# Kernel optimization log

Hardware: AMD Instinct MI355X
Metric: run time of the kernel (lower is better)

Reference implementation:

```python
import jax, jax.numpy as jnp
import numpy as np

# --- model constants (match init_kwargs / Mamba2 defaults) ---
NUM_BLOCKS = 2
D_MODEL = 768
EXPAND = 2
D_INNER = EXPAND * D_MODEL          # 1536
D_STATE = 128
D_CONV = 4
HEADDIM = 64
NHEADS = D_INNER // HEADDIM         # 24
CONV_DIM = D_INNER + 2 * D_STATE    # 1792 (x, B, C go through the depthwise conv)
D_IN_PROJ = 2 * D_INNER + 2 * D_STATE + NHEADS  # 3352
VOCAB = 32000
LABEL_DIM = 1000
EPS = 1e-5


def _layernorm(x, w, b):
    mu = jnp.mean(x, axis=-1, keepdims=True)
    var = jnp.mean(jnp.square(x - mu), axis=-1, keepdims=True)
    return (x - mu) * jax.lax.rsqrt(var + EPS) * w + b


def _dwconv_causal(x, w, b):
    # x: [B, L, C], w: [C, K] depthwise kernel, b: [C]
    C, K = w.shape
    xt = jnp.transpose(x, (0, 2, 1))  # [B, C, L]
    out = jax.lax.conv_general_dilated(
        xt, w[:, None, :], window_strides=(1,), padding=[(K - 1, 0)],
        feature_group_count=C, dimension_numbers=("NCH", "OIH", "NCH"))
    return jnp.transpose(out, (0, 2, 1)) + b


def _ssd_scan(xh, Bm, Cm, dt, A):
    # xh: [B,L,H,P], Bm/Cm: [B,L,N], dt: [B,L,H], A: [H]
    Bsz, L, H, P = xh.shape
    N = Bm.shape[-1]
    dA = jnp.exp(dt * A)  # [B,L,H], in (0,1)

    def step(h, inp):
        xt, bt, ct, dat, dtt = inp  # [B,H,P],[B,N],[B,N],[B,H],[B,H]
        h = h * dat[:, :, None, None] + (dtt[:, :, None, None] * xt[..., None]) * bt[:, None, None, :]
        y = jnp.einsum('bhpn,bn->bhp', h, ct)
        return h, y

    h0 = jnp.zeros((Bsz, H, P, N), dtype=xh.dtype)
    xs = (jnp.transpose(xh, (1, 0, 2, 3)),
          jnp.transpose(Bm, (1, 0, 2)),
          jnp.transpose(Cm, (1, 0, 2)),
          jnp.transpose(dA, (1, 0, 2)),
          jnp.transpose(dt, (1, 0, 2)))
    _, ys = jax.lax.scan(step, h0, xs)  # ys: [L,B,H,P]
    return jnp.transpose(ys, (1, 0, 2, 3))


def _mamba2(x, Win, conv_w, conv_b, dt_bias, A_log, Dp, rms_w, Wout):
    Bsz, L, _ = x.shape
    zxbcdt = x @ Win  # [B,L,D_IN_PROJ]
    z = zxbcdt[..., :D_INNER]
    xBC = zxbcdt[..., D_INNER:D_INNER + CONV_DIM]
    dt = zxbcdt[..., D_INNER + CONV_DIM:]  # [B,L,H]
    dt = jax.nn.softplus(dt + dt_bias)

    xBC = jax.nn.silu(_dwconv_causal(xBC, conv_w, conv_b))
    xs = xBC[..., :D_INNER]
    Bm = xBC[..., D_INNER:D_INNER + D_STATE]
    Cm = xBC[..., D_INNER + D_STATE:]

    xh = xs.reshape(Bsz, L, NHEADS, HEADDIM)
    A = -jnp.exp(A_log)  # [H]
    y = _ssd_scan(xh, Bm, Cm, dt, A) + Dp[None, None, :, None] * xh  # [B,L,H,P]
    y = y.reshape(Bsz, L, D_INNER)

    # gated RMSNorm: norm(y * silu(z)) * weight
    y = y * jax.nn.silu(z)
    y = y * jax.lax.rsqrt(jnp.mean(jnp.square(y), axis=-1, keepdims=True) + EPS) * rms_w
    return y @ Wout


def _forward(tokens, emb, ln_w, ln_b, Win, conv_w, conv_b, dt_bias, A_log, Dp, rms_w, Wout, Wcls, bcls):
    x = emb[tokens]  # [B,L,D_MODEL]
    for i in range(NUM_BLOCKS):
        nx = _layernorm(x, ln_w[i], ln_b[i])
        x = x + _mamba2(nx, Win[i], conv_w[i], conv_b[i], dt_bias[i],
                        A_log[i], Dp[i], rms_w[i], Wout[i])
        # dropout_rate=0 (eval) -> identity; use_glu=False -> no post stage
    return x @ Wcls + bcls


def setup_inputs() -> dict:
    key = jax.random.key(0)
    ks = jax.random.split(key, 12)
    B, L = 2, 512
    tokens = jax.random.randint(ks[0], (B, L), 0, VOCAB)
    emb = jax.random.normal(ks[1], (VOCAB, D_MODEL), jnp.float32) * 0.02
    ln_w = jnp.ones((NUM_BLOCKS, D_MODEL), jnp.float32)
    ln_b = jnp.zeros((NUM_BLOCKS, D_MODEL), jnp.float32)
    Win = jax.random.normal(ks[2], (NUM_BLOCKS, D_MODEL, D_IN_PROJ), jnp.float32) / np.sqrt(D_MODEL)
    conv_w = jax.random.normal(ks[3], (NUM_BLOCKS, CONV_DIM, D_CONV), jnp.float32) / np.sqrt(D_CONV)
    conv_b = jnp.zeros((NUM_BLOCKS, CONV_DIM), jnp.float32)
    dt0 = jax.random.uniform(ks[4], (NUM_BLOCKS, NHEADS), jnp.float32, 1e-3, 0.1)
    dt_bias = dt0 + jnp.log(-jnp.expm1(-dt0))  # inverse softplus
    A_log = jnp.log(jax.random.uniform(ks[5], (NUM_BLOCKS, NHEADS), jnp.float32, 1.0, 16.0))
    Dp = jnp.ones((NUM_BLOCKS, NHEADS), jnp.float32)
    rms_w = jnp.ones((NUM_BLOCKS, D_INNER), jnp.float32)
    Wout = jax.random.normal(ks[6], (NUM_BLOCKS, D_INNER, D_MODEL), jnp.float32) / np.sqrt(D_INNER)
    Wcls = jax.random.normal(ks[7], (D_MODEL, LABEL_DIM), jnp.float32) / np.sqrt(D_MODEL)
    bcls = jnp.zeros((LABEL_DIM,), jnp.float32)
    return {"tokens": tokens, "emb": emb, "ln_w": ln_w, "ln_b": ln_b, "Win": Win,
            "conv_w": conv_w, "conv_b": conv_b, "dt_bias": dt_bias, "A_log": A_log,
            "Dp": Dp, "rms_w": rms_w, "Wout": Wout, "Wcls": Wcls, "bcls": bcls}


def reference(tokens, emb, ln_w, ln_b, Win, conv_w, conv_b, dt_bias, A_log, Dp, rms_w, Wout, Wcls, bcls):
    return _forward(tokens, emb, ln_w, ln_b, Win, conv_w, conv_b, dt_bias, A_log, Dp, rms_w, Wout, Wcls, bcls)
```

## Files before the change

kernel.cpp:

```cpp
#include <hip/hip_runtime.h>
#include <hip/hip_bf16.h>
#include <math.h>

#define B_SZ 2
#define L_SEQ 512
#define DMODEL 768
#define DINNER 1536
#define DSTATE 128
#define HEADDIM 64
#define NHEADS 24
#define CONVDIM 1792
#define DINPROJ 3352
#define ROWS (B_SZ * L_SEQ)

#define CHUNK 32
#define NCHUNK (L_SEQ / CHUNK)
#define BCDIM (2 * DSTATE)

#define NPAD_IN 3456
#define NPAD_CLS 1024

typedef __attribute__((ext_vector_type(8))) __bf16 bf16x8;
typedef __attribute__((ext_vector_type(4))) __bf16 bf16x4;
typedef __attribute__((ext_vector_type(4))) float f32x4;

typedef __attribute__((address_space(1))) const unsigned int as1_u32;
typedef __attribute__((address_space(3))) unsigned int as3_u32;

__device__ __forceinline__ void gload16(const void* g, void* s) {
  __builtin_amdgcn_global_load_lds((as1_u32*)(unsigned long)g, (as3_u32*)(unsigned long)s, 16, 0,
                                   0);
}

__device__ __forceinline__ float siluf(float x) { return x / (1.f + expf(-x)); }
__device__ __forceinline__ float softplusf(float x) {
  return x > 0.f ? x + log1pf(expf(-x)) : log1pf(expf(x));
}

__device__ __forceinline__ float block_reduce_sum(float v, float* sred) {
  int tid = threadIdx.x;
  for (int off = 32; off; off >>= 1) v += __shfl_down(v, off, 64);
  int wid = tid >> 6, lane = tid & 63;
  if (lane == 0) sred[wid] = v;
  __syncthreads();
  float total;
  if (tid == 0) {
    total = 0.f;
    int nw = blockDim.x >> 6;
    for (int i = 0; i < nw; ++i) total += sred[i];
    sred[0] = total;
  }
  __syncthreads();
  total = sred[0];
  __syncthreads();
  return total;
}

__global__ __launch_bounds__(256) void decomp_all_kernel(
    const float* __restrict__ Win, const float* __restrict__ Wout,
    const float* __restrict__ Wcls, const int* __restrict__ tok, const float* __restrict__ emb,
    const float* __restrict__ lnw0, const float* __restrict__ lnb0, float* __restrict__ x,
    __bf16* __restrict__ nxh, __bf16* __restrict__ nxl, __bf16* __restrict__ wih0,
    __bf16* __restrict__ wil0, __bf16* __restrict__ wih1, __bf16* __restrict__ wil1,
    __bf16* __restrict__ woh0, __bf16* __restrict__ wol0, __bf16* __restrict__ woh1,
    __bf16* __restrict__ wol1, __bf16* __restrict__ wch, __bf16* __restrict__ wcl) {
  constexpr int TIN = (NPAD_IN / 32) * (DMODEL / 32);
  constexpr int TOUT = (DMODEL / 32) * (DINNER / 32);
  constexpr int TCLS = (NPAD_CLS / 32) * (DMODEL / 32);
  __shared__ float tile[32][33];
  int bid = blockIdx.x;
  int tid = threadIdx.x;

  if (bid >= 2 * TIN + 2 * TOUT + TCLS) {
    int row = bid - (2 * TIN + 2 * TOUT + TCLS);
    int t = tok[row];
    float v[3];
    float s = 0.f;
#pragma unroll
    for (int j = 0; j < 3; ++j) {
      v[j] = emb[(size_t)t * DMODEL + tid + j * 256];
      s += v[j];
      x[(size_t)row * DMODEL + tid + j * 256] = v[j];
    }
    float* sred = (float*)tile;
    float mean = block_reduce_sum(s, sred) * (1.f / DMODEL);
    float s2 = 0.f;
#pragma unroll
    for (int j = 0; j < 3; ++j) {
      float d = v[j] - mean;
      s2 += d * d;
    }
    float var = block_reduce_sum(s2, sred) * (1.f / DMODEL);
    float r = 1.f / sqrtf(var + 1e-5f);
#pragma unroll
    for (int j = 0; j < 3; ++j) {
      int d = tid + j * 256;
      float val = (v[j] - mean) * r * lnw0[d] + lnb0[d];
      __bf16 h = (__bf16)val;
      nxh[(size_t)row * DMODEL + d] = h;
      nxl[(size_t)row * DMODEL + d] = (__bf16)(val - (float)h);
    }
    return;
  }

  const float* W;
  __bf16 *Th, *Tl;
  int K, N, ntx, r;
  if (bid < TIN) {
    W = Win; Th = wih0; Tl = wil0; K = DMODEL; N = DINPROJ; ntx = NPAD_IN / 32; r = bid;
  } else if (bid < 2 * TIN) {
    W = Win + (size_t)DMODEL * DINPROJ; Th = wih1; Tl = wil1; K = DMODEL; N = DINPROJ;
    ntx = NPAD_IN / 32; r = bid - TIN;
  } else if (bid < 2 * TIN + TOUT) {
    W = Wout; Th = woh0; Tl = wol0; K = DINNER; N = DMODEL; ntx = DMODEL / 32; r = bid - 2 * TIN;
  } else if (bid < 2 * TIN + 2 * TOUT) {
    W = Wout + (size_t)DINNER * DMODEL; Th = woh1; Tl = wol1; K = DINNER; N = DMODEL;
    ntx = DMODEL / 32; r = bid - 2 * TIN - TOUT;
  } else {
    W = Wcls; Th = wch; Tl = wcl; K = DMODEL; N = 1000; ntx = NPAD_CLS / 32;
    r = bid - 2 * TIN - 2 * TOUT;
  }
  int bn = (r % ntx) * 32, bk = (r / ntx) * 32;

  int i = tid >> 3, j4 = (tid & 7) * 4;
  int kk = bk + i;
  int nn = bn + j4;
  float4 v;
  if (nn + 3 < N) {
    v = *(const float4*)(W + (size_t)kk * N + nn);
  } else {
    v.x = (nn + 0 < N) ? W[(size_t)kk * N + nn + 0] : 0.f;
    v.y = (nn + 1 < N) ? W[(size_t)kk * N + nn + 1] : 0.f;
    v.z = (nn + 2 < N) ? W[(size_t)kk * N + nn + 2] : 0.f;
    v.w = (nn + 3 < N) ? W[(size_t)kk * N + nn + 3] : 0.f;
  }
  tile[i][j4 + 0] = v.x;
  tile[i][j4 + 1] = v.y;
  tile[i][j4 + 2] = v.z;
  tile[i][j4 + 3] = v.w;
  __syncthreads();
  int n = bn + i;
  bf16x4 hv, lv;
#pragma unroll
  for (int q = 0; q < 4; ++q) {
    float f = tile[j4 + q][i];
    __bf16 h = (__bf16)f;
    hv[q] = h;
    lv[q] = (__bf16)(f - (float)h);
  }
  *(bf16x4*)(Th + (size_t)n * K + bk + j4) = hv;
  *(bf16x4*)(Tl + (size_t)n * K + bk + j4) = lv;
}

__global__ __launch_bounds__(256) void ln_kernel(const float* __restrict__ x,
                                                 const float* __restrict__ w,
                                                 const float* __restrict__ b,
                                                 __bf16* __restrict__ oh,
                                                 __bf16* __restrict__ ol) {
  __shared__ float sred[8];
  int row = blockIdx.x, tid = threadIdx.x;
  const float* xr = x + (size_t)row * DMODEL;
  float v[3];
  float s = 0.f;
#pragma unroll
  for (int j = 0; j < 3; ++j) {
    v[j] = xr[tid + j * 256];
    s += v[j];
  }
  float mean = block_reduce_sum(s, sred) * (1.f / DMODEL);
  float s2 = 0.f;
#pragma unroll
  for (int j = 0; j < 3; ++j) {
    float d = v[j] - mean;
    s2 += d * d;
  }
  float var = block_reduce_sum(s2, sred) * (1.f / DMODEL);
  float r = 1.f / sqrtf(var + 1e-5f);
#pragma unroll
  for (int j = 0; j < 3; ++j) {
    int d = tid + j * 256;
    float val = (v[j] - mean) * r * w[d] + b[d];
    __bf16 h = (__bf16)val;
    oh[(size_t)row * DMODEL + d] = h;
    ol[(size_t)row * DMODEL + d] = (__bf16)(val - (float)h);
  }
}

__global__ __launch_bounds__(256) void act_decomp_kernel(const float* __restrict__ x,
                                                         __bf16* __restrict__ oh,
                                                         __bf16* __restrict__ ol) {
  int row = blockIdx.x, tid = threadIdx.x;
#pragma unroll
  for (int j = 0; j < 3; ++j) {
    int d = tid + j * 256;
    float v = x[(size_t)row * DMODEL + d];
    __bf16 h = (__bf16)v;
    oh[(size_t)row * DMODEL + d] = h;
    ol[(size_t)row * DMODEL + d] = (__bf16)(v - (float)h);
  }
}

template <int FM, int FN, bool ATOMIC>
__global__ __launch_bounds__(256) void mfma_gemm_kernel(
    const __bf16* __restrict__ Ahi, const __bf16* __restrict__ Alo,
    const __bf16* __restrict__ Bhi, const __bf16* __restrict__ Blo,
    const float* __restrict__ addsrc, const float* __restrict__ bias, float* __restrict__ C,
    int N, int K, int kslice, int nbx, int nwg) {
  constexpr int BM = FM * 32;
  constexpr int BN = FN * 32;
  constexpr int RGA = BM / 16;
  constexpr int RGB = BN / 16;
  constexpr int NITER = (2 * (RGA + RGB)) / 4;
  constexpr int ABYTES = BM * 64;
  constexpr int BBYTES = BN * 64;
  constexpr int BUFBYTES = 2 * ABYTES + 2 * BBYTES;
  __shared__ char lds[2 * BUFBYTES];

  int tid = threadIdx.x;
  int wave = tid >> 6, lane = tid & 63;
  int wm = wave >> 1, wn = wave & 1;
  int bx, by;
  if (nbx > 0) {
    int orig = (blockIdx.x % 8) * (nwg / 8) + blockIdx.x / 8;
    bx = orig % nbx;
    by = orig / nbx;
  } else {
    bx = blockIdx.x;
    by = blockIdx.y;
  }
  int bm = by * BM;
  int bn = bx * BN;
  int kbeg = ATOMIC ? blockIdx.z * kslice : 0;
  int kend = ATOMIC ? (kbeg + kslice) : K;
  int l2 = lane >> 2;
  int gch = (lane & 3) ^ ((lane >> 3) & 3);
  int lr = lane & 15, lg = lane >> 4;

  f32x4 acc[FM][FN] = {};

  auto stage = [&](char* buf, int k0) {
#pragma unroll
    for (int it = 0; it < NITER; ++it) {
      int rg = wave + it * 4;
      const __bf16* src;
      int row0, boff;
      if (rg < RGA) {
        src = Ahi;
        row0 = bm + rg * 16;
        boff = rg * 1024;
      } else if (rg < 2 * RGA) {
        src = Alo;
        row0 = bm + (rg - RGA) * 16;
        boff = ABYTES + (rg - RGA) * 1024;
      } else if (rg < 2 * RGA + RGB) {
        src = Bhi;
        row0 = bn + (rg - 2 * RGA) * 16;
        boff = 2 * ABYTES + (rg - 2 * RGA) * 1024;
      } else {
        src = Blo;
        row0 = bn + (rg - 2 * RGA - RGB) * 16;
        boff = 2 * ABYTES + BBYTES + (rg - 2 * RGA - RGB) * 1024;
      }
      gload16(src + (size_t)(row0 + l2) * K + k0 + gch * 8, buf + boff);
    }
  };

  stage(lds, kbeg);
  __syncthreads();

  char* curb = lds;
  char* nxtb = lds + BUFBYTES;
  for (int k0 = kbeg; k0 < kend; k0 += 32) {
    if (k0 + 32 < kend) stage(nxtb, k0 + 32);

    bf16x8 ahi[FM], alo[FM], bhi[FN], blo[FN];
#pragma unroll
    for (int m = 0; m < FM; ++m) {
      int r = wm * FM * 16 + m * 16 + lr;
      int off = r * 64 + ((lg ^ ((r >> 1) & 3)) * 16);
      ahi[m] = *(const bf16x8*)(curb + off);
      alo[m] = *(const bf16x8*)(curb + ABYTES + off);
    }
#pragma unroll
    for (int n = 0; n < FN; ++n) {
      int r = wn * FN * 16 + n * 16 + lr;
      int off = r * 64 + ((lg ^ ((r >> 1) & 3)) * 16);
      bhi[n] = *(const bf16x8*)(curb + 2 * ABYTES + off);
      blo[n] = *(const bf16x8*)(curb + 2 * ABYTES + BBYTES + off);
    }
#pragma unroll
    for (int m = 0; m < FM; ++m)
#pragma unroll
      for (int n = 0; n < FN; ++n) {
        acc[m][n] = __builtin_amdgcn_mfma_f32_16x16x32_bf16(ahi[m], bhi[n], acc[m][n], 0, 0, 0);
        acc[m][n] = __builtin_amdgcn_mfma_f32_16x16x32_bf16(ahi[m], blo[n], acc[m][n], 0, 0, 0);
        acc[m][n] = __builtin_amdgcn_mfma_f32_16x16x32_bf16(alo[m], bhi[n], acc[m][n], 0, 0, 0);
      }
    __syncthreads();
    char* t = curb;
    curb = nxtb;
    nxtb = t;
  }

#pragma unroll
  for (int m = 0; m < FM; ++m) {
#pragma unroll
    for (int n = 0; n < FN; ++n) {
      int gcol = bn + wn * FN * 16 + n * 16 + lr;
      if (gcol < N) {
#pragma unroll
        for (int r = 0; r < 4; ++r) {
          int grow = bm + wm * FM * 16 + m * 16 + lg * 4 + r;
          if (ATOMIC) {
            unsafeAtomicAdd(&C[(size_t)grow * N + gcol], acc[m][n][r]);
          } else {
            float v = acc[m][n][r];
            if (addsrc) v += addsrc[(size_t)grow * N + gcol];
            if (bias) v += bias[gcol];
            C[(size_t)grow * N + gcol] = v;
          }
        }
      }
    }
  }
}

__global__ __launch_bounds__(256) void convBC_kernel(const float* __restrict__ zx,
                                                     const float* __restrict__ cw,
                                                     const float* __restrict__ cb,
                                                     const float* __restrict__ dtb,
                                                     float* __restrict__ xBC,
                                                     float* __restrict__ dts) {
  int row = blockIdx.x;
  int c = threadIdx.x;
  int ch = DINNER + c;
  int l = row & (L_SEQ - 1);
  float acc = cb[ch];
#pragma unroll
  for (int k = 0; k < 4; ++k) {
    int ls = l - 3 + k;
    if (ls >= 0)
      acc = fmaf(cw[ch * 4 + k], zx[(size_t)(row - 3 + k) * DINPROJ + DINNER + ch], acc);
  }
  xBC[(size_t)row * BCDIM + c] = siluf(acc);
  if (c < NHEADS) {
    float raw = zx[(size_t)row * DINPROJ + DINNER + CONVDIM + c] + dtb[c];
    dts[(size_t)row * NHEADS + c] = softplusf(raw);
  }
}

__global__ __launch_bounds__(256) void sraw_kernel(const float* __restrict__ xBC,
                                                   float* __restrict__ Sraw) {
  __shared__ float Bs[CHUNK][132];
  __shared__ float Cs[CHUNK][132];
  int ci = blockIdx.x, b = blockIdx.y;
  int tid = threadIdx.x;
  int row0 = b * L_SEQ + ci * CHUNK;
#pragma unroll
  for (int i = 0; i < 4; ++i) {
    int vi = tid + i * 256;
    int t = vi >> 5;
    int n4 = (vi & 31) * 4;
    const float* r = xBC + (size_t)(row0 + t) * BCDIM;
    *(float4*)&Bs[t][n4] = *(const float4*)(r + n4);
    *(float4*)&Cs[t][n4] = *(const float4*)(r + DSTATE + n4);
  }
  __syncthreads();
  int t0 = (tid >> 4) * 2;
  int s0 = (tid & 15) * 2;
  float sacc[2][2] = {};
#pragma unroll
  for (int n = 0; n < DSTATE; n += 4) {
    float cr[2][4], br[2][4];
#pragma unroll
    for (int i = 0; i < 2; ++i) *(float4*)&cr[i][0] = *(const float4*)&Cs[t0 + i][n];
#pragma unroll
    for (int j = 0; j < 2; ++j) *(float4*)&br[j][0] = *(const float4*)&Bs[s0 + j][n];
#pragma unroll
    for (int i = 0; i < 2; ++i)
#pragma unroll
      for (int j = 0; j < 2; ++j)
#pragma unroll
        for (int k = 0; k < 4; ++k) sacc[i][j] = fmaf(cr[i][k], br[j][k], sacc[i][j]);
  }
  float* Sp = Sraw + ((size_t)(b * NCHUNK + ci) * CHUNK) * CHUNK;
#pragma unroll
  for (int i = 0; i < 2; ++i)
#pragma unroll
    for (int j = 0; j < 2; ++j) Sp[(t0 + i) * CHUNK + s0 + j] = sacc[i][j];
}

__global__ __launch_bounds__(256) void chunk_local_kernel(
    const float* __restrict__ zx, const float* __restrict__ xBC, const float* __restrict__ Sraw,
    const float* __restrict__ dts, const float* __restrict__ cw, const float* __restrict__ cb,
    const float* __restrict__ Alog, const float* __restrict__ Dp, float* __restrict__ y,
    __bf16* __restrict__ G, float* __restrict__ et, float* __restrict__ elast) {
  __shared__ float Bs[CHUNK][132];
  __shared__ float Xs[CHUNK][68];
  __shared__ float Ss[CHUNK][36];
  __shared__ float sP[CHUNK], sW[CHUNK], sDt[CHUNK];

  int ci = blockIdx.x, h = blockIdx.y, b = blockIdx.z;
  int bh = b * NHEADS + h;
  int tid = threadIdx.x;
  int row0 = b * L_SEQ + ci * CHUNK;

#pragma unroll
  for (int i = 0; i < 2; ++i) {
    int vi = tid + i * 256;
    int t = vi >> 4;
    int n8 = (vi & 15) * 8;
    const float* r = xBC + (size_t)(row0 + t) * BCDIM;
    *(float4*)&Bs[t][n8] = *(const float4*)(r + n8);
    *(float4*)&Bs[t][n8 + 4] = *(const float4*)(r + n8 + 4);
  }
#pragma unroll
  for (int i = 0; i < 2; ++i) {
    int vi = tid + i * 256;
    int t = vi >> 4;
    int p4 = (vi & 15) * 4;
    int cX = h * HEADDIM + p4;
    float oX[4];
#pragma unroll
    for (int q = 0; q < 4; ++q) oX[q] = cb[cX + q];
#pragma unroll
    for (int k = 0; k < 4; ++k) {
      if (ci > 0 || t + k >= 3) {
        float4 v = *(const float4*)(zx + (size_t)(row0 + t - 3 + k) * DINPROJ + DINNER + cX);
#pragma unroll
        for (int q = 0; q < 4; ++q) oX[q] = fmaf(cw[(cX + q) * 4 + k], ((const float*)&v)[q], oX[q]);
      }
    }
#pragma unroll
    for (int q = 0; q < 4; ++q) Xs[t][p4 + q] = siluf(oX[q]);
  }
  if (tid < 32) {
    int t = tid;
    float Ah = -expf(Alog[h]);
    float dtv = dts[(size_t)(row0 + t) * NHEADS + h];
    float P = dtv * Ah;
#pragma unroll
    for (int off = 1; off < 32; off <<= 1) {
      float u = __shfl_up(P, off, 32);
      if (t >= off) P += u;
    }
    float Plast = __shfl(P, 31, 32);
    float e = expf(P);
    sP[t] = P;
    sDt[t] = dtv;
    sW[t] = expf(Plast - P) * dtv;
    et[(size_t)(bh * NCHUNK + ci) * CHUNK + t] = e;
    if (t == 31) elast[bh * NCHUNK + ci] = e;
  }
  __syncthreads();

  int t0 = (tid >> 4) * 2;
  int s0 = (tid & 15) * 2;
  {
    const float* Sp = Sraw + ((size_t)(b * NCHUNK + ci) * CHUNK) * CHUNK;
#pragma unroll
    for (int i = 0; i < 2; ++i)
#pragma unroll
      for (int j = 0; j < 2; ++j) {
        int t = t0 + i, s = s0 + j;
        float sr = Sp[t * CHUNK + s];
        Ss[t][s] = (t >= s) ? sr * expf(sP[t] - sP[s]) * sDt[s] : 0.f;
      }
  }
  __syncthreads();

  {
    int p0 = (tid & 15) * 4;
    float acc[2][4] = {};
#pragma unroll
    for (int s = 0; s < CHUNK; s += 4) {
      float sr[2][4], xr[4][4];
#pragma unroll
      for (int i = 0; i < 2; ++i) *(float4*)&sr[i][0] = *(const float4*)&Ss[t0 + i][s];
#pragma unroll
      for (int u = 0; u < 4; ++u) *(float4*)&xr[u][0] = *(const float4*)&Xs[s + u][p0];
#pragma unroll
      for (int i = 0; i < 2; ++i)
#pragma unroll
        for (int j = 0; j < 4; ++j)
#pragma unroll
          for (int u = 0; u < 4; ++u) acc[i][j] = fmaf(sr[i][u], xr[u][j], acc[i][j]);
    }
    float Dh = Dp[h];
#pragma unroll
    for (int i = 0; i < 2; ++i) {
      int row = row0 + t0 + i;
      float4 o;
      o.x = acc[i][0] + Dh * Xs[t0 + i][p0 + 0];
      o.y = acc[i][1] + Dh * Xs[t0 + i][p0 + 1];
      o.z = acc[i][2] + Dh * Xs[t0 + i][p0 + 2];
      o.w = acc[i][3] + Dh * Xs[t0 + i][p0 + 3];
      *(float4*)(y + (size_t)row * DINNER + h * HEADDIM + p0) = o;
    }
  }

  {
    int n0 = (tid >> 4) * 8;
    int p0 = (tid & 15) * 4;
    float g[8][4] = {};
#pragma unroll 4
    for (int s = 0; s < CHUNK; ++s) {
      float w = sW[s];
      float bv[8], xv[4];
      *(float4*)&bv[0] = *(const float4*)&Bs[s][n0];
      *(float4*)&bv[4] = *(const float4*)&Bs[s][n0 + 4];
      *(float4*)&xv[0] = *(const float4*)&Xs[s][p0];
#pragma unroll
      for (int k = 0; k < 8; ++k) {
        float wb = w * bv[k];
#pragma unroll
        for (int j = 0; j < 4; ++j) g[k][j] = fmaf(wb, xv[j], g[k][j]);
      }
    }
    __bf16* Gp = G + ((size_t)bh * NCHUNK + ci) * (DSTATE * HEADDIM);
#pragma unroll
    for (int k = 0; k < 8; ++k) {
      bf16x4 o;
#pragma unroll
      for (int q = 0; q < 4; ++q) o[q] = (__bf16)g[k][q];
      *(bf16x4*)(Gp + (size_t)(n0 + k) * HEADDIM + p0) = o;
    }
  }
}

__global__ __launch_bounds__(256) void combine_kernel(__bf16* __restrict__ G,
                                                      const float* __restrict__ elast) {
  int part = blockIdx.x;
  int bh = blockIdx.y;
  int gi = part * 256 + threadIdx.x;
  __bf16* base = G + (size_t)bh * NCHUNK * (DSTATE * HEADDIM);
  const float* el = elast + bh * NCHUNK;
  float h0 = 0.f, h1 = 0.f, h2 = 0.f, h3 = 0.f;
#pragma unroll
  for (int c = 0; c < NCHUNK - 1; ++c) {
    bf16x4 g = *(bf16x4*)(base + (size_t)c * (DSTATE * HEADDIM) + gi * 4);
    float e = el[c];
    h0 = fmaf(e, h0, (float)g[0]);
    h1 = fmaf(e, h1, (float)g[1]);
    h2 = fmaf(e, h2, (float)g[2]);
    h3 = fmaf(e, h3, (float)g[3]);
    bf16x4 o;
    o[0] = (__bf16)h0;
    o[1] = (__bf16)h1;
    o[2] = (__bf16)h2;
    o[3] = (__bf16)h3;
    *(bf16x4*)(base + (size_t)c * (DSTATE * HEADDIM) + gi * 4) = o;
  }
}

__global__ __launch_bounds__(256) void apply_inter_kernel(const float* __restrict__ xBC,
                                                          const __bf16* __restrict__ G,
                                                          const float* __restrict__ et,
                                                          float* __restrict__ y) {
  __shared__ float Cs[CHUNK][132];
  __shared__ float Hs[DSTATE][68];
  __shared__ float sE[CHUNK];
  int ci = blockIdx.x + 1;
  int h = blockIdx.y, b = blockIdx.z;
  int bh = b * NHEADS + h;
  int tid = threadIdx.x;
  int row0 = b * L_SEQ + ci * CHUNK;

#pragma unroll
  for (int i = 0; i < 4; ++i) {
    int vi = tid + i * 256;
    int t = vi >> 5;
    int n4 = (vi & 31) * 4;
    *(float4*)&Cs[t][n4] = *(const float4*)(xBC + (size_t)(row0 + t) * BCDIM + DSTATE + n4);
  }
  const __bf16* Hsrc = G + ((size_t)bh * NCHUNK + (ci - 1)) * (DSTATE * HEADDIM);
#pragma unroll
  for (int i = 0; i < 8; ++i) {
    int vi = tid + i * 256;
    int n = vi >> 4;
    int p4 = (vi & 15) * 4;
    bf16x4 g = *(const bf16x4*)(Hsrc + (size_t)n * HEADDIM + p4);
#pragma unroll
    for (int q = 0; q < 4; ++q) Hs[n][p4 + q] = (float)g[q];
  }
  if (tid < CHUNK) sE[tid] = et[(size_t)(bh * NCHUNK + ci) * CHUNK + tid];
  __syncthreads();

  int t0 = (tid >> 4) * 2;
  int p0 = (tid & 15) * 4;
  float acc[2][4] = {};
#pragma unroll
  for (int n = 0; n < DSTATE; n += 4) {
    float cr[2][4], hr[4][4];
#pragma unroll
    for (int i = 0; i < 2; ++i) *(float4*)&cr[i][0] = *(const float4*)&Cs[t0 + i][n];
#pragma unroll
    for (int u = 0; u < 4; ++u) *(float4*)&hr[u][0] = *(const float4*)&Hs[n + u][p0];
#pragma unroll
    for (int i = 0; i < 2; ++i)
#pragma unroll
      for (int j = 0; j < 4; ++j)
#pragma unroll
        for (int u = 0; u < 4; ++u) acc[i][j] = fmaf(cr[i][u], hr[u][j], acc[i][j]);
  }
#pragma unroll
  for (int i = 0; i < 2; ++i) {
    int row = row0 + t0 + i;
    float e = sE[t0 + i];
    float* yp = y + (size_t)row * DINNER + h * HEADDIM + p0;
    float4 cur = *(float4*)yp;
    cur.x = fmaf(e, acc[i][0], cur.x);
    cur.y = fmaf(e, acc[i][1], cur.y);
    cur.z = fmaf(e, acc[i][2], cur.z);
    cur.w = fmaf(e, acc[i][3], cur.w);
    *(float4*)yp = cur;
  }
}

__global__ __launch_bounds__(256) void gate_rms_kernel(const float* __restrict__ y,
                                                       const float* __restrict__ zx,
                                                       const float* __restrict__ rmsw,
                                                       __bf16* __restrict__ oh,
                                                       __bf16* __restrict__ ol) {
  __shared__ float sred[8];
  int row = blockIdx.x, tid = threadIdx.x;
  const float* z = zx + (size_t)row * DINPROJ;
  const float* yr = y + (size_t)row * DINNER;
  float v[6];
  float ss = 0.f;
#pragma unroll
  for (int j = 0; j < 6; ++j) {
    int d = tid + j * 256;
    float val = yr[d] * siluf(z[d]);
    v[j] = val;
    ss += val * val;
  }
  float total = block_reduce_sum(ss, sred);
  float r = 1.f / sqrtf(total * (1.f / DINNER) + 1e-5f);
#pragma unroll
  for (int j = 0; j < 6; ++j) {
    int d = tid + j * 256;
    float val = v[j] * r * rmsw[d];
    __bf16 h = (__bf16)val;
    oh[(size_t)row * DINNER + d] = h;
    ol[(size_t)row * DINNER + d] = (__bf16)(val - (float)h);
  }
}

extern "C" void kernel_launch(void* const* d_in, const int* in_sizes, int n_in,
                              void* d_out, int out_size, void* d_ws, size_t ws_size,
                              hipStream_t stream) {
  const int* tokens = (const int*)d_in[0];
  const float* emb = (const float*)d_in[1];
  const float* ln_w = (const float*)d_in[2];
  const float* ln_b = (const float*)d_in[3];
  const float* Win = (const float*)d_in[4];
  const float* conv_w = (const float*)d_in[5];
  const float* conv_b = (const float*)d_in[6];
  const float* dt_bias = (const float*)d_in[7];
  const float* A_log = (const float*)d_in[8];
  const float* Dp = (const float*)d_in[9];
  const float* rms_w = (const float*)d_in[10];
  const float* Wout = (const float*)d_in[11];
  const float* Wcls = (const float*)d_in[12];
  const float* bcls = (const float*)d_in[13];
  float* out = (float*)d_out;

  float* ws = (float*)d_ws;
  float* x = ws;
  float* zx = x + (size_t)ROWS * DMODEL;
  float* y = zx + (size_t)ROWS * DINPROJ;
  __bf16* G = (__bf16*)(y + (size_t)ROWS * DINNER);
  float* et = (float*)(G + (size_t)B_SZ * NHEADS * NCHUNK * DSTATE * HEADDIM);
  float* elast = et + (size_t)B_SZ * NHEADS * NCHUNK * CHUNK;
  float* xBC = elast + B_SZ * NHEADS * NCHUNK;
  float* Sraw = xBC + (size_t)ROWS * BCDIM;
  float* dts = Sraw + (size_t)B_SZ * NCHUNK * CHUNK * CHUNK;
  __bf16* bp = (__bf16*)(dts + (size_t)ROWS * NHEADS);
  __bf16* nxh = bp;  bp += (size_t)ROWS * DMODEL;
  __bf16* nxl = bp;  bp += (size_t)ROWS * DMODEL;
  __bf16* yh = bp;   bp += (size_t)ROWS * DINNER;
  __bf16* yl = bp;   bp += (size_t)ROWS * DINNER;
  __bf16* xh = bp;   bp += (size_t)ROWS * DMODEL;
  __bf16* xl = bp;   bp += (size_t)ROWS * DMODEL;
  __bf16* wih0 = bp; bp += (size_t)NPAD_IN * DMODEL;
  __bf16* wil0 = bp; bp += (size_t)NPAD_IN * DMODEL;
  __bf16* wih1 = bp; bp += (size_t)NPAD_IN * DMODEL;
  __bf16* wil1 = bp; bp += (size_t)NPAD_IN * DMODEL;
  __bf16* woh0 = bp; bp += (size_t)DMODEL * DINNER;
  __bf16* wol0 = bp; bp += (size_t)DMODEL * DINNER;
  __bf16* woh1 = bp; bp += (size_t)DMODEL * DINNER;
  __bf16* wol1 = bp; bp += (size_t)DMODEL * DINNER;
  __bf16* wch = bp;  bp += (size_t)NPAD_CLS * DMODEL;
  __bf16* wcl = bp;

  constexpr int TIN = (NPAD_IN / 32) * (DMODEL / 32);
  constexpr int TOUT = (DMODEL / 32) * (DINNER / 32);
  constexpr int TCLS = (NPAD_CLS / 32) * (DMODEL / 32);
  decomp_all_kernel<<<2 * TIN + 2 * TOUT + TCLS + ROWS, 256, 0, stream>>>(
      Win, Wout, Wcls, tokens, emb, ln_w, ln_b, x, nxh, nxl, wih0, wil0, wih1, wil1, woh0, wol0,
      woh1, wol1, wch, wcl);

  for (int blk = 0; blk < 2; ++blk) {
    const float* cw_b = conv_w + (size_t)blk * CONVDIM * 4;
    const float* cb_b = conv_b + (size_t)blk * CONVDIM;
    const float* dtb_b = dt_bias + (size_t)blk * NHEADS;
    const float* Alog_b = A_log + (size_t)blk * NHEADS;
    const float* Dp_b = Dp + (size_t)blk * NHEADS;
    const float* rmsw_b = rms_w + (size_t)blk * DINNER;
    __bf16* wih = blk ? wih1 : wih0;
    __bf16* wil = blk ? wil1 : wil0;
    __bf16* woh = blk ? woh1 : woh0;
    __bf16* wol = blk ? wol1 : wol0;

    if (blk == 1) {
      ln_kernel<<<ROWS, 256, 0, stream>>>(x, ln_w + (size_t)blk * DMODEL,
                                          ln_b + (size_t)blk * DMODEL, nxh, nxl);
    }

    mfma_gemm_kernel<2, 2, false><<<(NPAD_IN / 64) * (ROWS / 64), 256, 0, stream>>>(
        nxh, nxl, wih, wil, nullptr, nullptr, zx, DINPROJ, DMODEL, 0, NPAD_IN / 64,
        (NPAD_IN / 64) * (ROWS / 64));

    convBC_kernel<<<ROWS, BCDIM, 0, stream>>>(zx, cw_b, cb_b, dtb_b, xBC, dts);

    sraw_kernel<<<dim3(NCHUNK, B_SZ), 256, 0, stream>>>(xBC, Sraw);

    chunk_local_kernel<<<dim3(NCHUNK, NHEADS, B_SZ), 256, 0, stream>>>(
        zx, xBC, Sraw, dts, cw_b, cb_b, Alog_b, Dp_b, y, G, et, elast);

    combine_kernel<<<dim3(8, B_SZ * NHEADS), 256, 0, stream>>>(G, elast);

    apply_inter_kernel<<<dim3(NCHUNK - 1, NHEADS, B_SZ), 256, 0, stream>>>(xBC, G, et, y);

    gate_rms_kernel<<<ROWS, 256, 0, stream>>>(y, zx, rmsw_b, yh, yl);

    mfma_gemm_kernel<2, 2, true><<<dim3(DMODEL / 64, ROWS / 64, 4), 256, 0, stream>>>(
        yh, yl, woh, wol, nullptr, nullptr, x, DMODEL, DINNER, DINNER / 4, 0, 0);
  }

  act_decomp_kernel<<<ROWS, 256, 0, stream>>>(x, xh, xl);
  mfma_gemm_kernel<2, 2, false><<<(NPAD_CLS / 64) * (ROWS / 64), 256, 0, stream>>>(
      xh, xl, wch, wcl, nullptr, bcls, out, 1000, DMODEL, 0, NPAD_CLS / 64,
      (NPAD_CLS / 64) * (ROWS / 64));
}
```

Baseline: 249.2 us.

## Fuse B/C depthwise conv into Sraw kernel and remap GEMM tile order

Merges the B/C causal conv, SiLU and dt softplus kernel into the chunk Sraw kernel, so each chunk block computes its conv outputs with a sliding register window and writes them straight into shared memory. This removes one launch and the global round trip for xBC before Sraw. It also changes the swizzled GEMM block mapping so consecutive work-groups walk down M instead of across N, which changes L2 reuse. The fused kernel runs only 32 blocks, which do the conv serially over 32 timesteps, so it gives up parallelism compared with the per-row 1024-block launch.

```diff
diff --git a/kernel.cpp b/kernel.cpp
--- a/kernel.cpp
+++ b/kernel.cpp
@@ -222,8 +222,9 @@
   int bx, by;
   if (nbx > 0) {
     int orig = (blockIdx.x % 8) * (nwg / 8) + blockIdx.x / 8;
-    bx = orig % nbx;
-    by = orig / nbx;
+    int nby = nwg / nbx;
+    bx = orig / nby;
+    by = orig % nby;
   } else {
     bx = blockIdx.x;
     by = blockIdx.y;
@@ -325,47 +326,42 @@
   }
 }
 
-__global__ __launch_bounds__(256) void convBC_kernel(const float* __restrict__ zx,
-                                                     const float* __restrict__ cw,
-                                                     const float* __restrict__ cb,
-                                                     const float* __restrict__ dtb,
-                                                     float* __restrict__ xBC,
-                                                     float* __restrict__ dts) {
-  int row = blockIdx.x;
-  int c = threadIdx.x;
-  int ch = DINNER + c;
-  int l = row & (L_SEQ - 1);
-  float acc = cb[ch];
-#pragma unroll
-  for (int k = 0; k < 4; ++k) {
-    int ls = l - 3 + k;
-    if (ls >= 0)
-      acc = fmaf(cw[ch * 4 + k], zx[(size_t)(row - 3 + k) * DINPROJ + DINNER + ch], acc);
-  }
-  xBC[(size_t)row * BCDIM + c] = siluf(acc);
-  if (c < NHEADS) {
-    float raw = zx[(size_t)row * DINPROJ + DINNER + CONVDIM + c] + dtb[c];
-    dts[(size_t)row * NHEADS + c] = softplusf(raw);
-  }
-}
-
-__global__ __launch_bounds__(256) void sraw_kernel(const float* __restrict__ xBC,
-                                                   float* __restrict__ Sraw) {
+__global__ __launch_bounds__(256) void convBC_sraw_kernel(
+    const float* __restrict__ zx, const float* __restrict__ cw, const float* __restrict__ cb,
+    const float* __restrict__ dtb, float* __restrict__ xBC, float* __restrict__ dts,
+    float* __restrict__ Sraw) {
   __shared__ float Bs[CHUNK][132];
   __shared__ float Cs[CHUNK][132];
   int ci = blockIdx.x, b = blockIdx.y;
   int tid = threadIdx.x;
   int row0 = b * L_SEQ + ci * CHUNK;
-#pragma unroll
-  for (int i = 0; i < 4; ++i) {
-    int vi = tid + i * 256;
-    int t = vi >> 5;
-    int n4 = (vi & 31) * 4;
-    const float* r = xBC + (size_t)(row0 + t) * BCDIM;
-    *(float4*)&Bs[t][n4] = *(const float4*)(r + n4);
-    *(float4*)&Cs[t][n4] = *(const float4*)(r + DSTATE + n4);
-  }
-  __syncthreads();
+  int c = tid;
+  int ch = DINNER + c;
+  int zcol = DINNER + ch;
+  float w0 = cw[ch * 4 + 0], w1 = cw[ch * 4 + 1], w2 = cw[ch * 4 + 2], w3 = cw[ch * 4 + 3];
+  float bias = cb[ch];
+  float x0 = 0.f, x1 = 0.f, x2 = 0.f;
+  if (ci > 0) {
+    x0 = zx[(size_t)(row0 - 3) * DINPROJ + zcol];
+    x1 = zx[(size_t)(row0 - 2) * DINPROJ + zcol];
+    x2 = zx[(size_t)(row0 - 1) * DINPROJ + zcol];
+  }
+  for (int t = 0; t < CHUNK; ++t) {
+    float x3 = zx[(size_t)(row0 + t) * DINPROJ + zcol];
+    float acc = fmaf(w3, x3, fmaf(w2, x2, fmaf(w1, x1, fmaf(w0, x0, bias))));
+    float v = siluf(acc);
+    if (c < DSTATE) Bs[t][c] = v;
+    else Cs[t][c - DSTATE] = v;
+    xBC[(size_t)(row0 + t) * BCDIM + c] = v;
+    x0 = x1; x1 = x2; x2 = x3;
+  }
+  for (int i = tid; i < CHUNK * NHEADS; i += 256) {
+    int t = i / NHEADS, h = i % NHEADS;
+    float raw = zx[(size_t)(row0 + t) * DINPROJ + DINNER + CONVDIM + h] + dtb[h];
+    dts[(size_t)(row0 + t) * NHEADS + h] = softplusf(raw);
+  }
+  __syncthreads();
+
   int t0 = (tid >> 4) * 2;
   int s0 = (tid & 15) * 2;
   float sacc[2][2] = {};
@@ -722,9 +718,8 @@
         nxh, nxl, wih, wil, nullptr, nullptr, zx, DINPROJ, DMODEL, 0, NPAD_IN / 64,
         (NPAD_IN / 64) * (ROWS / 64));
 
-    convBC_kernel<<<ROWS, BCDIM, 0, stream>>>(zx, cw_b, cb_b, dtb_b, xBC, dts);
-
-    sraw_kernel<<<dim3(NCHUNK, B_SZ), 256, 0, stream>>>(xBC, Sraw);
+    convBC_sraw_kernel<<<dim3(NCHUNK, B_SZ), 256, 0, stream>>>(zx, cw_b, cb_b, dtb_b, xBC, dts,
+                                                               Sraw);
 
     chunk_local_kernel<<<dim3(NCHUNK, NHEADS, B_SZ), 256, 0, stream>>>(
         zx, xBC, Sraw, dts, cw_b, cb_b, Alog_b, Dp_b, y, G, et, elast);
```

Measured after the change: 259.5 us. 1.04x slower.
